# Kernel tuning notes

Hardware: AMD Instinct MI355X
Metric: run time of the kernel (lower is better)

The kernel has to match this reference:

```python
import jax, jax.numpy as jnp
import numpy as np

N_PEDS = 4096
GRID_N = 16          # grid is GRID_N x GRID_N cells
CELL_SIDE = 0.6      # meters per cell
POOL_DIM = 2         # DIRECTIONAL pooling: relative (vx, vy)
OUT_DIM = 256
H_DIM = 128
AREA = 20.0          # scene is AREA x AREA meters


def setup_inputs() -> dict:
    key = jax.random.key(0)
    k1, k2, k3, k4, k5 = jax.random.split(key, 5)
    positions = jax.random.uniform(k1, (N_PEDS, 2), dtype=jnp.float32) * AREA
    # past position = current minus a small per-step displacement (~pedestrian velocity)
    past_positions = positions - jax.random.normal(k2, (N_PEDS, 2), dtype=jnp.float32) * 0.4
    h = jax.random.normal(k3, (N_PEDS, H_DIM), dtype=jnp.float32)
    in_dim = GRID_N * GRID_N * POOL_DIM
    scale = 1.0 / np.sqrt(in_dim)
    W_emb = jax.random.uniform(k4, (OUT_DIM, in_dim), dtype=jnp.float32, minval=-scale, maxval=scale)
    b_emb = jax.random.uniform(k5, (OUT_DIM,), dtype=jnp.float32, minval=-scale, maxval=scale)
    return {"h": h, "positions": positions, "past_positions": past_positions,
            "W_emb": W_emb, "b_emb": b_emb}


def _directional_grid(positions, past_positions):
    """DIRECTIONAL grid pooling: bin neighbours' relative velocities into an
    n x n grid (cell_side meters per cell) centred on each pedestrian, averaging
    contributions per cell (norm_cell=True). Returns [N, n*n, 2]."""
    n = GRID_N
    num = positions.shape[0]
    vel = positions - past_positions                         # [N, 2]
    rel_pos = positions[None, :, :] - positions[:, None, :]  # [N, N, 2] pos_j - pos_i
    rel_vel = vel[None, :, :] - vel[:, None, :]              # [N, N, 2] vel_j - vel_i
    # cell indices: floor(rel/cell + n/2)
    oij = jnp.floor(rel_pos / CELL_SIDE + n / 2).astype(jnp.int32)  # [N, N, 2]
    in_range = jnp.all((oij >= 0) & (oij < n), axis=-1)             # [N, N]
    valid = in_range & ~jnp.eye(num, dtype=bool)                    # exclude self
    cell_idx = jnp.where(valid, oij[..., 0] * n + oij[..., 1], 0)   # [N, N]
    vals = jnp.where(valid[..., None], rel_vel, 0.0)                # [N, N, 2]
    rows = jnp.arange(num)[:, None]                                 # [N, 1]
    grid = jnp.zeros((num, n * n, POOL_DIM), dtype=positions.dtype)
    grid = grid.at[rows, cell_idx].add(vals)                        # scatter-add values
    cnt = jnp.zeros((num, n * n), dtype=positions.dtype)
    cnt = cnt.at[rows, cell_idx].add(valid.astype(positions.dtype)) # occupancy counts
    grid = grid / jnp.maximum(cnt, 1.0)[..., None]                  # norm_cell: mean per cell
    return grid


def reference(h, positions, past_positions, W_emb, b_emb):
    grid = _directional_grid(positions, past_positions)      # [N, n*n, 2]
    flat = grid.reshape(grid.shape[0], -1)                   # [N, n*n*2]
    return jax.nn.relu(flat @ W_emb.T + b_emb)               # [N, out_dim]
```

## Files before the change

### kernel.cpp

```cpp
#include <hip/hip_runtime.h>

typedef __attribute__((ext_vector_type(4))) float f32x4;
typedef __attribute__((ext_vector_type(8))) short bf16x8;

#define NP 4096
#define IB 2

__device__ __forceinline__ unsigned short f2bf(float f) {
  unsigned int u = __float_as_uint(f);
  u = u + 0x7FFFu + ((u >> 16) & 1u);
  return (unsigned short)(u >> 16);
}

__global__ __launch_bounds__(256, 8) void pool_kernel(
    const float2* __restrict__ pos, const float2* __restrict__ past,
    unsigned short* __restrict__ gridws) {
  __shared__ unsigned long long acc[IB][256];
  const int tid = threadIdx.x;
  const int tx = tid & (IB - 1);
  const int ty = tid >> 1;
  const int ibase = blockIdx.x * IB;
  const int i = ibase + tx;

  for (int idx = tid; idx < IB * 256 * 2; idx += 256)
    ((unsigned int*)acc)[idx] = 0u;
  __syncthreads();

  const float2 pi = pos[i];
  const float2 qi = past[i];
  const float vix = pi.x - qi.x;
  const float viy = pi.y - qi.y;
  unsigned long long* accp = acc[tx];
  const float inv06 = 1.0f / 0.6f;

  auto process = [&](float2 pj, float2 qj) {
    float rx = pj.x - pi.x;
    float ry = pj.y - pi.y;
    float ax = __builtin_fmaf(rx, inv06, 8.0f);
    float ay = __builtin_fmaf(ry, inv06, 8.0f);
    bool unc = (fabsf(ax - rintf(ax)) < 1e-4f) |
               (fabsf(ay - rintf(ay)) < 1e-4f);
    float fx, fy;
    if (__any(unc)) {
      fx = floorf(rx / 0.6f + 8.0f);
      fy = floorf(ry / 0.6f + 8.0f);
    } else {
      fx = floorf(ax);
      fy = floorf(ay);
    }
    int ix = (int)fx;
    int iy = (int)fy;
    if (((unsigned)ix < 16u) & ((unsigned)iy < 16u)) {
      float rvx = (pj.x - qj.x) - vix;
      float rvy = (pj.y - qj.y) - viy;
      unsigned int qx = (unsigned int)((int)rintf(rvx * 2048.0f) + 16384);
      unsigned int qy = (unsigned int)((int)rintf(rvy * 2048.0f) + 16384);
      unsigned long long p = ((unsigned long long)qx << 38) |
                             ((unsigned long long)qy << 12) | 1ull;
      atomicAdd(&accp[(ix << 4) + iy], p);
    }
  };

  for (int jo = 0; jo < NP; jo += 512) {
    int j0 = jo + ty;
    float2 p0 = pos[j0];        float2 q0 = past[j0];
    float2 p1 = pos[j0 + 128];  float2 q1 = past[j0 + 128];
    float2 p2 = pos[j0 + 256];  float2 q2 = past[j0 + 256];
    float2 p3 = pos[j0 + 384];  float2 q3 = past[j0 + 384];
    process(p0, q0);
    process(p1, q1);
    process(p2, q2);
    process(p3, q3);
  }
  __syncthreads();

  const int cell = tid;
  const float selfc = (cell == 136) ? 1.0f : 0.0f;
#pragma unroll
  for (int il = 0; il < IB; ++il) {
    unsigned long long raw = acc[il][cell];
    unsigned int cnt = (unsigned int)(raw & 0xFFFull);
    int sxq = (int)((unsigned int)(raw >> 38)) - (int)(cnt << 14);
    int syq = (int)((unsigned int)((raw >> 12) & 0x3FFFFFFull)) - (int)(cnt << 14);
    float cn = (float)cnt - selfc;
    float d = fmaxf(cn, 1.0f);
    float sx = (float)sxq * (1.0f / 2048.0f);
    float sy = (float)syq * (1.0f / 2048.0f);
    unsigned int packed =
        ((unsigned int)f2bf(sy / d) << 16) | (unsigned int)f2bf(sx / d);
    *(unsigned int*)&gridws[(size_t)(ibase + il) * 512 + cell * 2] = packed;
  }
}

__global__ __launch_bounds__(256) void gemm_kernel(
    const unsigned short* __restrict__ A, const float* __restrict__ W,
    const float* __restrict__ bias, float* __restrict__ out) {
  __shared__ unsigned short As[64][40];
  __shared__ unsigned short Bs[64][40];
  const int tid = threadIdx.x;
  const int lane = tid & 63;
  const int wid = tid >> 6;
  const int wr = wid >> 1;
  const int wc = wid & 1;
  const int mbase = blockIdx.y * 64;
  const int nbase = blockIdx.x * 64;
  const int srow = tid >> 2;
  const int skq = tid & 3;

  f32x4 acc00 = {0.f, 0.f, 0.f, 0.f};
  f32x4 acc01 = {0.f, 0.f, 0.f, 0.f};
  f32x4 acc10 = {0.f, 0.f, 0.f, 0.f};
  f32x4 acc11 = {0.f, 0.f, 0.f, 0.f};

  const int lrow = lane & 15;
  const int lk = (lane >> 4) * 8;

  for (int kb = 0; kb < 512; kb += 32) {
    __syncthreads();
    *(bf16x8*)&As[srow][skq * 8] =
        *(const bf16x8*)&A[(size_t)(mbase + srow) * 512 + kb + skq * 8];
    const float* wp = &W[(size_t)(nbase + srow) * 512 + kb + skq * 8];
    float4 w0 = *(const float4*)wp;
    float4 w1 = *(const float4*)(wp + 4);
    bf16x8 bv;
    bv[0] = (short)f2bf(w0.x); bv[1] = (short)f2bf(w0.y);
    bv[2] = (short)f2bf(w0.z); bv[3] = (short)f2bf(w0.w);
    bv[4] = (short)f2bf(w1.x); bv[5] = (short)f2bf(w1.y);
    bv[6] = (short)f2bf(w1.z); bv[7] = (short)f2bf(w1.w);
    *(bf16x8*)&Bs[srow][skq * 8] = bv;
    __syncthreads();

    bf16x8 a0 = *(const bf16x8*)&As[wr * 32 + lrow][lk];
    bf16x8 a1 = *(const bf16x8*)&As[wr * 32 + 16 + lrow][lk];
    bf16x8 b0 = *(const bf16x8*)&Bs[wc * 32 + lrow][lk];
    bf16x8 b1 = *(const bf16x8*)&Bs[wc * 32 + 16 + lrow][lk];
    acc00 = __builtin_amdgcn_mfma_f32_16x16x32_bf16(a0, b0, acc00, 0, 0, 0);
    acc01 = __builtin_amdgcn_mfma_f32_16x16x32_bf16(a0, b1, acc01, 0, 0, 0);
    acc10 = __builtin_amdgcn_mfma_f32_16x16x32_bf16(a1, b0, acc10, 0, 0, 0);
    acc11 = __builtin_amdgcn_mfma_f32_16x16x32_bf16(a1, b1, acc11, 0, 0, 0);
  }

  const int row0 = mbase + wr * 32 + (lane >> 4) * 4;
  const int col0 = nbase + wc * 32 + lrow;
#pragma unroll
  for (int ni = 0; ni < 2; ++ni) {
    int col = col0 + ni * 16;
    float bv = bias[col];
    const f32x4* a0p = (ni == 0) ? &acc00 : &acc01;
    const f32x4* a1p = (ni == 0) ? &acc10 : &acc11;
#pragma unroll
    for (int q = 0; q < 4; ++q) {
      float v0 = (*a0p)[q] + bv;
      out[(size_t)(row0 + q) * 256 + col] = fmaxf(v0, 0.0f);
      float v1 = (*a1p)[q] + bv;
      out[(size_t)(row0 + 16 + q) * 256 + col] = fmaxf(v1, 0.0f);
    }
  }
}

extern "C" void kernel_launch(void* const* d_in, const int* in_sizes, int n_in,
                              void* d_out, int out_size, void* d_ws, size_t ws_size,
                              hipStream_t stream) {
  const float2* pos = (const float2*)d_in[1];
  const float2* past = (const float2*)d_in[2];
  const float* W = (const float*)d_in[3];
  const float* bias = (const float*)d_in[4];
  float* out = (float*)d_out;

  unsigned short* gridws = (unsigned short*)d_ws;

  pool_kernel<<<NP / IB, 256, 0, stream>>>(pos, past, gridws);
  dim3 g(256 / 64, NP / 64);
  gemm_kernel<<<g, 256, 0, stream>>>(gridws, W, bias, out);
}
```

Before: 35.86 us.

## Pre-convert weights to bf16 and load MFMA fragments directly from global memory

Adds a separate kernel that converts W to bf16 once per call into workspace, so the GEMM no longer converts fp32 weights inside its K loop. The GEMM drops shared memory and barriers. Each of two waves computes a 32x64 tile, loading A and B fragments straight from global memory and issuing 16 MFMAs per 64-wide K step. This adds a third kernel launch and per-lane strided global loads, in exchange for removing the LDS staging and sync overhead.

```diff
diff --git a/kernel.cpp b/kernel.cpp
--- a/kernel.cpp
+++ b/kernel.cpp
@@ -92,68 +92,66 @@
   }
 }
 
-__global__ __launch_bounds__(256) void gemm_kernel(
-    const unsigned short* __restrict__ A, const float* __restrict__ W,
+__global__ __launch_bounds__(256) void wconv_kernel(
+    const float* __restrict__ W, unsigned short* __restrict__ Wb) {
+  int i = (blockIdx.x * 256 + threadIdx.x) * 8;
+  float4 w0 = *(const float4*)&W[i];
+  float4 w1 = *(const float4*)&W[i + 4];
+  bf16x8 bv;
+  bv[0] = (short)f2bf(w0.x); bv[1] = (short)f2bf(w0.y);
+  bv[2] = (short)f2bf(w0.z); bv[3] = (short)f2bf(w0.w);
+  bv[4] = (short)f2bf(w1.x); bv[5] = (short)f2bf(w1.y);
+  bv[6] = (short)f2bf(w1.z); bv[7] = (short)f2bf(w1.w);
+  *(bf16x8*)&Wb[i] = bv;
+}
+
+__global__ __launch_bounds__(128) void gemm_kernel(
+    const unsigned short* __restrict__ A, const unsigned short* __restrict__ Wb,
     const float* __restrict__ bias, float* __restrict__ out) {
-  __shared__ unsigned short As[64][40];
-  __shared__ unsigned short Bs[64][40];
-  const int tid = threadIdx.x;
-  const int lane = tid & 63;
-  const int wid = tid >> 6;
-  const int wr = wid >> 1;
-  const int wc = wid & 1;
-  const int mbase = blockIdx.y * 64;
+  const int lane = threadIdx.x & 63;
+  const int w = threadIdx.x >> 6;
+  const int mbase = blockIdx.y * 64 + w * 32;
   const int nbase = blockIdx.x * 64;
-  const int srow = tid >> 2;
-  const int skq = tid & 3;
-
-  f32x4 acc00 = {0.f, 0.f, 0.f, 0.f};
-  f32x4 acc01 = {0.f, 0.f, 0.f, 0.f};
-  f32x4 acc10 = {0.f, 0.f, 0.f, 0.f};
-  f32x4 acc11 = {0.f, 0.f, 0.f, 0.f};
-
   const int lrow = lane & 15;
   const int lk = (lane >> 4) * 8;
 
-  for (int kb = 0; kb < 512; kb += 32) {
-    __syncthreads();
-    *(bf16x8*)&As[srow][skq * 8] =
-        *(const bf16x8*)&A[(size_t)(mbase + srow) * 512 + kb + skq * 8];
-    const float* wp = &W[(size_t)(nbase + srow) * 512 + kb + skq * 8];
-    float4 w0 = *(const float4*)wp;
-    float4 w1 = *(const float4*)(wp + 4);
-    bf16x8 bv;
-    bv[0] = (short)f2bf(w0.x); bv[1] = (short)f2bf(w0.y);
-    bv[2] = (short)f2bf(w0.z); bv[3] = (short)f2bf(w0.w);
-    bv[4] = (short)f2bf(w1.x); bv[5] = (short)f2bf(w1.y);
-    bv[6] = (short)f2bf(w1.z); bv[7] = (short)f2bf(w1.w);
-    *(bf16x8*)&Bs[srow][skq * 8] = bv;
-    __syncthreads();
+  f32x4 acc[2][4] = {};
 
-    bf16x8 a0 = *(const bf16x8*)&As[wr * 32 + lrow][lk];
-    bf16x8 a1 = *(const bf16x8*)&As[wr * 32 + 16 + lrow][lk];
-    bf16x8 b0 = *(const bf16x8*)&Bs[wc * 32 + lrow][lk];
-    bf16x8 b1 = *(const bf16x8*)&Bs[wc * 32 + 16 + lrow][lk];
-    acc00 = __builtin_amdgcn_mfma_f32_16x16x32_bf16(a0, b0, acc00, 0, 0, 0);
-    acc01 = __builtin_amdgcn_mfma_f32_16x16x32_bf16(a0, b1, acc01, 0, 0, 0);
-    acc10 = __builtin_amdgcn_mfma_f32_16x16x32_bf16(a1, b0, acc10, 0, 0, 0);
-    acc11 = __builtin_amdgcn_mfma_f32_16x16x32_bf16(a1, b1, acc11, 0, 0, 0);
+  for (int kb = 0; kb < 512; kb += 64) {
+    bf16x8 a[2][2], b[2][4];
+#pragma unroll
+    for (int ks = 0; ks < 2; ++ks) {
+      const int k0 = kb + ks * 32 + lk;
+#pragma unroll
+      for (int mf = 0; mf < 2; ++mf)
+        a[ks][mf] = *(const bf16x8*)&A[(size_t)(mbase + mf * 16 + lrow) * 512 + k0];
+#pragma unroll
+      for (int nf = 0; nf < 4; ++nf)
+        b[ks][nf] = *(const bf16x8*)&Wb[(size_t)(nbase + nf * 16 + lrow) * 512 + k0];
+    }
+#pragma unroll
+    for (int ks = 0; ks < 2; ++ks)
+#pragma unroll
+      for (int mf = 0; mf < 2; ++mf)
+#pragma unroll
+        for (int nf = 0; nf < 4; ++nf)
+          acc[mf][nf] = __builtin_amdgcn_mfma_f32_16x16x32_bf16(
+              a[ks][mf], b[ks][nf], acc[mf][nf], 0, 0, 0);
   }
 
-  const int row0 = mbase + wr * 32 + (lane >> 4) * 4;
-  const int col0 = nbase + wc * 32 + lrow;
+  const int rq = (lane >> 4) * 4;
 #pragma unroll
-  for (int ni = 0; ni < 2; ++ni) {
-    int col = col0 + ni * 16;
-    float bv = bias[col];
-    const f32x4* a0p = (ni == 0) ? &acc00 : &acc01;
-    const f32x4* a1p = (ni == 0) ? &acc10 : &acc11;
+  for (int nf = 0; nf < 4; ++nf) {
+    const int col = nbase + nf * 16 + lrow;
+    const float bv = bias[col];
 #pragma unroll
-    for (int q = 0; q < 4; ++q) {
-      float v0 = (*a0p)[q] + bv;
-      out[(size_t)(row0 + q) * 256 + col] = fmaxf(v0, 0.0f);
-      float v1 = (*a1p)[q] + bv;
-      out[(size_t)(row0 + 16 + q) * 256 + col] = fmaxf(v1, 0.0f);
+    for (int mf = 0; mf < 2; ++mf) {
+      const int row0 = mbase + mf * 16 + rq;
+#pragma unroll
+      for (int q = 0; q < 4; ++q) {
+        float v = acc[mf][nf][q] + bv;
+        out[(size_t)(row0 + q) * 256 + col] = fmaxf(v, 0.0f);
+      }
     }
   }
 }
@@ -168,8 +166,10 @@
   float* out = (float*)d_out;
 
   unsigned short* gridws = (unsigned short*)d_ws;
+  unsigned short* Wb = (unsigned short*)((char*)d_ws + 4 * 1024 * 1024);
 
+  wconv_kernel<<<(256 * 512) / (256 * 8), 256, 0, stream>>>(W, Wb);
   pool_kernel<<<NP / IB, 256, 0, stream>>>(pos, past, gridws);
   dim3 g(256 / 64, NP / 64);
-  gemm_kernel<<<g, 256, 0, stream>>>(gridws, W, bias, out);
+  gemm_kernel<<<g, 128, 0, stream>>>(gridws, Wb, bias, out);
 }
```

Result: slower. 41.20 us (+14.9%).
